# Performance work log

Measured on AMD Instinct MI355X. Metric: run time of the kernel, lower is better.

## Reference

```python
import jax, jax.numpy as jnp
import numpy as np

B, L, D_IN, D_EDGE, H, D = 2, 384, 256, 128, 8, 32
SCALE = D ** (-0.5)


def setup_inputs() -> dict:
    key = jax.random.key(0)
    ks = jax.random.split(key, 12)
    hd = H * D
    s_in = D_IN ** -0.5
    s_e = D_EDGE ** -0.5
    return {
        "node_feat": jax.random.normal(ks[0], (B, L, D_IN), jnp.float32),
        "edge_feat": jax.random.normal(ks[1], (B, L, L, D_EDGE), jnp.float32),
        "edge_mask": (jax.random.uniform(ks[2], (B, L, L)) > 0.15).astype(jnp.float32),
        "Wq": jax.random.normal(ks[3], (D_IN, hd), jnp.float32) * s_in,
        "bq": jnp.zeros((hd,), jnp.float32),
        "Wk": jax.random.normal(ks[4], (D_IN, hd), jnp.float32) * s_in,
        "bk": jnp.zeros((hd,), jnp.float32),
        "Wv": jax.random.normal(ks[5], (D_IN, hd), jnp.float32) * s_in,
        "bv": jnp.zeros((hd,), jnp.float32),
        "We": jax.random.normal(ks[6], (D_EDGE, hd), jnp.float32) * s_e,
        "Wu": jax.random.normal(ks[7], (D_IN, hd), jnp.float32) * s_in,
        "bu": jnp.zeros((hd,), jnp.float32),
    }


def _split_heads(t):
    # (b, l, h*d) -> (b, h, l, d)
    b, l, _ = t.shape
    return t.reshape(b, l, H, D).transpose(0, 2, 1, 3)


def reference(node_feat, edge_feat, edge_mask, Wq, bq, Wk, bk, Wv, bv, We, Wu, bu):
    q = _split_heads(node_feat @ Wq + bq)
    k = _split_heads(node_feat @ Wk + bk)
    v = _split_heads(node_feat @ Wv + bv)
    # edge embedding: (b, i, j, h*d) -> (b, h, i, j, d)
    b, l = edge_feat.shape[0], edge_feat.shape[1]
    e = (edge_feat @ We).reshape(b, l, l, H, D).transpose(0, 3, 1, 2, 4)
    logit = jnp.einsum('bhid,bhjd->bhij', q, k)
    logit = logit + jnp.einsum('bhid,bhijd->bhij', q, e)
    att = logit * SCALE
    att = att + ((1.0 - edge_mask) * -1e9)[:, None, :, :]
    att = jax.nn.softmax(att, axis=-1)  # dropout is identity in eval / p=0
    updated = jnp.einsum('bhij,bhjd->bhid', att, v)
    updated = updated + jnp.einsum('bhij,bhijd->bhid', att, e)
    updated = updated.transpose(0, 2, 1, 3).reshape(b, l, H * D)
    return (node_feat @ Wu + bu) + updated
```

## Files before the change

kernel.cpp:

```cpp
#include <hip/hip_runtime.h>
#include <cstdint>

#define NB 2
#define LL 384
#define DIN 256
#define DE 128
#define NH 8
#define DH 32
#define HD 256
#define SCALE 0.17677669529663687f

typedef __attribute__((ext_vector_type(8))) short bf16x8;
typedef __attribute__((ext_vector_type(4))) float f32x4;

static __device__ __forceinline__ unsigned short f2bf(float f) {
    uint32_t u = __builtin_bit_cast(uint32_t, f);
    u += 0x7FFF + ((u >> 16) & 1);
    return (unsigned short)(u >> 16);
}
static __device__ __forceinline__ float bf2f(unsigned short u) {
    return __builtin_bit_cast(float, (uint32_t)u << 16);
}
static __device__ __forceinline__ float getf4(const float4& v, int k) {
    return k == 0 ? v.x : k == 1 ? v.y : k == 2 ? v.z : v.w;
}
static __device__ __forceinline__ bf16x8 pack8(const float4& a, const float4& b) {
    bf16x8 p;
    p[0]=(short)f2bf(a.x); p[1]=(short)f2bf(a.y); p[2]=(short)f2bf(a.z); p[3]=(short)f2bf(a.w);
    p[4]=(short)f2bf(b.x); p[5]=(short)f2bf(b.y); p[6]=(short)f2bf(b.z); p[7]=(short)f2bf(b.w);
    return p;
}

__global__ __launch_bounds__(128) void prep_we(const float* __restrict__ We,
                                               unsigned short* __restrict__ WeT) {
    const int n = blockIdx.x;
    const int k = threadIdx.x;
    WeT[n * DE + k] = f2bf(We[(size_t)k * HD + n]);
}

__global__ __launch_bounds__(256) void proj_kernel(
    const float* __restrict__ node,
    const float* __restrict__ Wq, const float* __restrict__ bq,
    const float* __restrict__ Wk, const float* __restrict__ bk,
    const float* __restrict__ Wv, const float* __restrict__ bv,
    const float* __restrict__ Wu, const float* __restrict__ bu,
    unsigned short* __restrict__ qb16, unsigned short* __restrict__ kb16,
    float* __restrict__ vb, float* __restrict__ ub)
{
    __shared__ __align__(16) float rows[4][DIN];
    const int t  = threadIdx.x;
    const int r0 = blockIdx.x * 4;

    #pragma unroll
    for (int r = 0; r < 4; ++r)
        rows[r][t] = node[(size_t)(r0 + r) * DIN + t];
    __syncthreads();

    float aq[4], ak[4], av[4], au[4];
    {
        const float vq = bq[t], vk = bk[t], vv = bv[t], vu = bu[t];
        #pragma unroll
        for (int r = 0; r < 4; ++r) { aq[r] = vq; ak[r] = vk; av[r] = vv; au[r] = vu; }
    }

    for (int f4 = 0; f4 < DIN / 4; ++f4) {
        float4 xv[4];
        #pragma unroll
        for (int r = 0; r < 4; ++r)
            xv[r] = *(const float4*)&rows[r][f4 * 4];
        #pragma unroll
        for (int k = 0; k < 4; ++k) {
            const int f = f4 * 4 + k;
            const float wq = Wq[(size_t)f * HD + t];
            const float wk = Wk[(size_t)f * HD + t];
            const float wv = Wv[(size_t)f * HD + t];
            const float wu = Wu[(size_t)f * HD + t];
            #pragma unroll
            for (int r = 0; r < 4; ++r) {
                const float x = getf4(xv[r], k);
                aq[r] += x * wq; ak[r] += x * wk; av[r] += x * wv; au[r] += x * wu;
            }
        }
    }

    #pragma unroll
    for (int r = 0; r < 4; ++r) {
        const size_t o = (size_t)(r0 + r) * HD + t;
        qb16[o] = f2bf(aq[r]); kb16[o] = f2bf(ak[r]);
        vb[o] = av[r]; ub[o] = au[r];
    }
}

__global__ __launch_bounds__(256) void vt_kernel(const float* __restrict__ vb,
                                                 unsigned short* __restrict__ vT) {
    __shared__ float tile[64][65];
    int blk = blockIdx.x;
    const int b  = blk / 24; blk %= 24;
    const int jt = blk / 4;
    const int ct = blk % 4;
    const int j0 = jt * 64, c0 = ct * 64;
    const int t  = threadIdx.x;
    const int c  = t & 63, j4 = t >> 6;
    #pragma unroll
    for (int rr = 0; rr < 16; ++rr) {
        const int j = j4 + 4 * rr;
        tile[j][c] = vb[(size_t)(b * LL + j0 + j) * HD + c0 + c];
    }
    __syncthreads();
    const int jj = t & 63, c4 = t >> 6;
    #pragma unroll
    for (int rr = 0; rr < 16; ++rr) {
        const int cc = c4 + 4 * rr;
        vT[(size_t)(b * HD + c0 + cc) * LL + j0 + jj] = f2bf(tile[jj][cc]);
    }
}

__global__ __launch_bounds__(256) void qk_kernel(
    const unsigned short* __restrict__ qb16, const unsigned short* __restrict__ kb16,
    const float* __restrict__ mask, float* __restrict__ logit_pre)
{
    int idx = blockIdx.x;
    const int jt = idx % 6; idx /= 6;
    const int it = idx % 6; idx /= 6;
    const int h  = idx % NH;
    const int b  = idx / NH;
    const int t    = threadIdx.x;
    const int lane = t & 63;
    const int w    = t >> 6;
    const int lid  = lane & 15;
    const int g    = lane >> 4;
    const int i0 = it * 64 + w * 16;
    const int j0 = jt * 64;

    const bf16x8 afr = *(const bf16x8*)&qb16[(size_t)(b * LL + i0 + lid) * HD + h * DH + g * 8];
    f32x4 acc[4];
    #pragma unroll
    for (int jj = 0; jj < 4; ++jj) {
        const bf16x8 bfrg = *(const bf16x8*)&kb16[(size_t)(b * LL + j0 + jj * 16 + lid) * HD + h * DH + g * 8];
        acc[jj] = __builtin_amdgcn_mfma_f32_16x16x32_bf16(afr, bfrg, (f32x4){0.f,0.f,0.f,0.f}, 0, 0, 0);
    }
    #pragma unroll
    for (int jj = 0; jj < 4; ++jj) {
        #pragma unroll
        for (int r = 0; r < 4; ++r) {
            const int i = i0 + 4 * g + r;
            const int j = j0 + jj * 16 + lid;
            const float lg = SCALE * acc[jj][r]
                           + (1.0f - mask[(size_t)(b * LL + i) * LL + j]) * -1e9f;
            logit_pre[((size_t)(b * NH + h) * LL + i) * LL + j] = lg;
        }
    }
}

__global__ __launch_bounds__(256) void qwe_kernel(
    const unsigned short* __restrict__ qb16, const unsigned short* __restrict__ WeT,
    unsigned short* __restrict__ qWe)
{
    const int bi = blockIdx.x;
    const int t  = threadIdx.x;
    const int h  = t >> 5;
    const int c0 = (t & 31) * 4;

    float qv[32];
    const unsigned short* qp = &qb16[(size_t)bi * HD + h * DH];
    #pragma unroll
    for (int d = 0; d < 32; ++d) qv[d] = bf2f(qp[d]);

    float acc0 = 0.f, acc1 = 0.f, acc2 = 0.f, acc3 = 0.f;
    #pragma unroll
    for (int d = 0; d < 32; ++d) {
        const ushort4 wt = *(const ushort4*)&WeT[(size_t)(h * DH + d) * DE + c0];
        acc0 += qv[d] * bf2f(wt.x); acc1 += qv[d] * bf2f(wt.y);
        acc2 += qv[d] * bf2f(wt.z); acc3 += qv[d] * bf2f(wt.w);
    }
    unsigned short* o = &qWe[(size_t)bi * (NH * DE) + h * DE + c0];
    o[0] = f2bf(SCALE * acc0); o[1] = f2bf(SCALE * acc1);
    o[2] = f2bf(SCALE * acc2); o[3] = f2bf(SCALE * acc3);
}

__global__ __launch_bounds__(256) void elog_kernel(
    const float* __restrict__ edge,
    const unsigned short* __restrict__ qWe,
    float* __restrict__ lpre)
{
    int idx = blockIdx.x;
    const int jt = idx % 3; idx /= 3;
    const int bi = idx;
    const int b = bi / LL, ii = bi % LL;
    const int t = threadIdx.x, lane = t & 63, w = t >> 6;
    const int lid = lane & 15, g = lane >> 4;
    const int hq = lid & 7;
    const int j0 = jt * 128 + w * 32;

    bf16x8 bfr[4];
    const unsigned short* qwp = &qWe[(size_t)bi * (NH * DE) + hq * DE];
    #pragma unroll
    for (int kt = 0; kt < 4; ++kt)
        bfr[kt] = *(const bf16x8*)&qwp[kt * 32 + g * 8];

    f32x4 acc[2];
    #pragma unroll
    for (int mt = 0; mt < 2; ++mt) {
        acc[mt] = (f32x4){0.f, 0.f, 0.f, 0.f};
        const float* ef = edge + ((size_t)bi * LL + j0 + mt * 16 + lid) * DE;
        #pragma unroll
        for (int kt = 0; kt < 4; ++kt) {
            const float4 x0 = *(const float4*)&ef[kt * 32 + g * 8];
            const float4 x1 = *(const float4*)&ef[kt * 32 + g * 8 + 4];
            acc[mt] = __builtin_amdgcn_mfma_f32_16x16x32_bf16(pack8(x0, x1), bfr[kt], acc[mt], 0, 0, 0);
        }
    }

    if (lid < 8) {
        float* lrow = lpre + ((size_t)(b * NH + hq) * LL + ii) * LL;
        #pragma unroll
        for (int mt = 0; mt < 2; ++mt) {
            float4* p4 = (float4*)&lrow[j0 + mt * 16 + 4 * g];
            float4 x = *p4;
            x.x += acc[mt][0]; x.y += acc[mt][1];
            x.z += acc[mt][2]; x.w += acc[mt][3];
            *p4 = x;
        }
    }
}

__global__ __launch_bounds__(256) void smax_kernel(
    const float* __restrict__ lpre, unsigned short* __restrict__ attb)
{
    const int t = threadIdx.x, lane = t & 63, w = t >> 6;
    const int row = blockIdx.x * 4 + w;
    const float* lr = lpre + (size_t)row * LL;

    float2 x[3];
    #pragma unroll
    for (int k = 0; k < 3; ++k)
        x[k] = *(const float2*)&lr[2 * lane + 128 * k];

    float m = fmaxf(x[0].x, x[0].y);
    m = fmaxf(m, fmaxf(x[1].x, x[1].y));
    m = fmaxf(m, fmaxf(x[2].x, x[2].y));
    #pragma unroll
    for (int off = 1; off < 64; off <<= 1) m = fmaxf(m, __shfl_xor(m, off));

    float p[6], s = 0.f;
    #pragma unroll
    for (int k = 0; k < 3; ++k) {
        p[2 * k]     = __expf(x[k].x - m);
        p[2 * k + 1] = __expf(x[k].y - m);
        s += p[2 * k] + p[2 * k + 1];
    }
    #pragma unroll
    for (int off = 1; off < 64; off <<= 1) s += __shfl_xor(s, off);
    const float inv = 1.0f / s;

    unsigned int* ao = (unsigned int*)attb + (size_t)row * (LL / 2);
    #pragma unroll
    for (int k = 0; k < 3; ++k) {
        const unsigned int pk = ((unsigned int)f2bf(p[2 * k + 1] * inv) << 16)
                              |  (unsigned int)f2bf(p[2 * k] * inv);
        ao[lane + 64 * k] = pk;
    }
}

__global__ __launch_bounds__(512, 4) void pvs_kernel(
    const float* __restrict__ edge,
    const unsigned short* __restrict__ attb,
    const unsigned short* __restrict__ vT,
    float* __restrict__ aEp,
    float* __restrict__ avp)
{
    int idx = blockIdx.x;
    const int jt = idx % 3; idx /= 3;
    const int bi = idx;
    const int b = bi / LL, ii = bi % LL;
    const int t = threadIdx.x, lane = t & 63, w = t >> 6;
    const int lid = lane & 15, g = lane >> 4;
    const int h = lid & 7;
    const int j0 = jt * 128;

    bf16x8 pA[4];
    const unsigned short* ab = attb + ((size_t)(b * NH + h) * LL + ii) * LL + j0;
    #pragma unroll
    for (int kt = 0; kt < 4; ++kt)
        pA[kt] = *(const bf16x8*)&ab[kt * 32 + g * 8];

    const float* Eb = edge + ((size_t)bi * LL + j0) * DE + w * 16 + lid;
    f32x4 accE = (f32x4){0.f, 0.f, 0.f, 0.f};
    #pragma unroll
    for (int kt = 0; kt < 4; ++kt) {
        bf16x8 be;
        #pragma unroll
        for (int u = 0; u < 8; ++u)
            be[u] = (short)f2bf(Eb[(size_t)(kt * 32 + g * 8 + u) * DE]);
        accE = __builtin_amdgcn_mfma_f32_16x16x32_bf16(pA[kt], be, accE, 0, 0, 0);
    }

    f32x4 accV[2];
    accV[0] = (f32x4){0.f, 0.f, 0.f, 0.f};
    accV[1] = (f32x4){0.f, 0.f, 0.f, 0.f};
    #pragma unroll
    for (int kt = 0; kt < 4; ++kt) {
        #pragma unroll
        for (int mt = 0; mt < 2; ++mt) {
            const bf16x8 vv = *(const bf16x8*)&vT[(size_t)(b * HD + w * DH + mt * 16 + lid) * LL + j0 + kt * 32 + g * 8];
            accV[mt] = __builtin_amdgcn_mfma_f32_16x16x32_bf16(pA[kt], vv, accV[mt], 0, 0, 0);
        }
    }

    float* aep = aEp + (size_t)(bi * 3 + jt) * (NH * DE);
    if (g < 2) {
        #pragma unroll
        for (int r = 0; r < 4; ++r)
            aep[(4 * g + r) * DE + w * 16 + lid] = accE[r];
    }
    float* avo = avp + (size_t)(bi * 3 + jt) * HD;
    #pragma unroll
    for (int mt = 0; mt < 2; ++mt)
        #pragma unroll
        for (int r = 0; r < 4; ++r)
            if (4 * g + r == w)
                avo[w * DH + mt * 16 + lid] = accV[mt][r];
}

__global__ __launch_bounds__(256) void finale_kernel(
    const float* __restrict__ aEp, const float* __restrict__ avp,
    const float* __restrict__ We,
    const float* __restrict__ ub,
    float* __restrict__ out)
{
    __shared__ float aEs[NH * DE];
    const int bi = blockIdx.x, t = threadIdx.x;

    #pragma unroll
    for (int q = 0; q < 4; ++q) {
        const int x = t + 256 * q;
        aEs[x] = aEp[(size_t)(bi * 3 + 0) * (NH * DE) + x]
               + aEp[(size_t)(bi * 3 + 1) * (NH * DE) + x]
               + aEp[(size_t)(bi * 3 + 2) * (NH * DE) + x];
    }
    __syncthreads();

    const int hd = t, h = hd >> 5;
    float acc = ub[(size_t)bi * HD + hd]
              + avp[(size_t)(bi * 3 + 0) * HD + hd]
              + avp[(size_t)(bi * 3 + 1) * HD + hd]
              + avp[(size_t)(bi * 3 + 2) * HD + hd];

    const float* sa = &aEs[h * DE];
    float a0 = 0.f, a1 = 0.f, a2 = 0.f, a3 = 0.f;
    #pragma unroll
    for (int c = 0; c < DE; c += 4) {
        a0 += sa[c]     * We[(size_t)(c)     * HD + hd];
        a1 += sa[c + 1] * We[(size_t)(c + 1) * HD + hd];
        a2 += sa[c + 2] * We[(size_t)(c + 2) * HD + hd];
        a3 += sa[c + 3] * We[(size_t)(c + 3) * HD + hd];
    }
    out[(size_t)bi * HD + hd] = acc + ((a0 + a1) + (a2 + a3));
}

extern "C" void kernel_launch(void* const* d_in, const int* in_sizes, int n_in,
                              void* d_out, int out_size, void* d_ws, size_t ws_size,
                              hipStream_t stream) {
    const float* node = (const float*)d_in[0];
    const float* edge = (const float*)d_in[1];
    const float* mask = (const float*)d_in[2];
    const float* Wq   = (const float*)d_in[3];
    const float* bq   = (const float*)d_in[4];
    const float* Wk   = (const float*)d_in[5];
    const float* bk   = (const float*)d_in[6];
    const float* Wv   = (const float*)d_in[7];
    const float* bv   = (const float*)d_in[8];
    const float* We   = (const float*)d_in[9];
    const float* Wu   = (const float*)d_in[10];
    const float* bu   = (const float*)d_in[11];
    float* out = (float*)d_out;

    const size_t rowsz = (size_t)NB * LL * HD;
    const size_t lsz   = (size_t)NB * NH * LL * LL;
    float* ws   = (float*)d_ws;
    float* vb   = ws;
    float* ubuf = vb + rowsz;
    float* lpre = ubuf + rowsz;
    float* aEp  = lpre + lsz;
    float* avp  = aEp + (size_t)NB * LL * 3 * NH * DE;
    unsigned short* us   = (unsigned short*)(avp + (size_t)NB * LL * 3 * HD);
    unsigned short* WeT  = us;
    unsigned short* qb16 = WeT + (size_t)HD * DE;
    unsigned short* kb16 = qb16 + rowsz;
    unsigned short* vT   = kb16 + rowsz;
    unsigned short* qWeB = vT + rowsz;
    unsigned short* attb = qWeB + (size_t)NB * LL * NH * DE;

    hipLaunchKernelGGL(prep_we, dim3(HD), dim3(DE), 0, stream, We, WeT);
    hipLaunchKernelGGL(proj_kernel, dim3(NB * LL / 4), dim3(256), 0, stream,
                       node, Wq, bq, Wk, bk, Wv, bv, Wu, bu, qb16, kb16, vb, ubuf);
    hipLaunchKernelGGL(vt_kernel, dim3(NB * (LL / 64) * (HD / 64)), dim3(256), 0, stream,
                       vb, vT);
    hipLaunchKernelGGL(qk_kernel, dim3(NB * NH * (LL / 64) * (LL / 64)), dim3(256), 0, stream,
                       qb16, kb16, mask, lpre);
    hipLaunchKernelGGL(qwe_kernel, dim3(NB * LL), dim3(256), 0, stream,
                       qb16, WeT, qWeB);
    hipLaunchKernelGGL(elog_kernel, dim3(NB * LL * 3), dim3(256), 0, stream,
                       edge, qWeB, lpre);
    hipLaunchKernelGGL(smax_kernel, dim3(NB * NH * LL / 4), dim3(256), 0, stream,
                       lpre, attb);
    hipLaunchKernelGGL(pvs_kernel, dim3(NB * LL * 3), dim3(512), 0, stream,
                       edge, attb, vT, aEp, avp);
    hipLaunchKernelGGL(finale_kernel, dim3(NB * LL), dim3(256), 0, stream,
                       aEp, avp, We, ubuf, out);
}
```

Baseline: 121.9 us.

## Emit transposed bf16 edge copy in logit kernel; read it in PV kernel

The edge-logit kernel now converts each edge tile to bf16, transposes it through swizzled shared memory, and writes a j-contiguous bf16 copy to workspace. The PV kernel then reads this half-size, coalesced copy instead of re-reading fp32 edge features with strided scalar loads. The PV kernel also drops to 256 threads, with each wave computing more output tiles, and the qk logit load is hoisted before the MFMAs. This trades an extra 75 MB-class bf16 write plus 32 KB of shared memory per block for a cheaper second pass over the edge tensor.

```diff
diff --git a/kernel.cpp b/kernel.cpp
--- a/kernel.cpp
+++ b/kernel.cpp
@@ -178,48 +178,88 @@
     o[2] = f2bf(SCALE * acc2); o[3] = f2bf(SCALE * acc3);
 }
 
-__global__ __launch_bounds__(256) void elog_kernel(
+__global__ __launch_bounds__(256, 2) void elog2_kernel(
     const float* __restrict__ edge,
     const unsigned short* __restrict__ qWe,
-    float* __restrict__ lpre)
-{
-    int idx = blockIdx.x;
-    const int jt = idx % 3; idx /= 3;
-    const int bi = idx;
+    float* __restrict__ lpre,
+    unsigned short* __restrict__ ebfT)
+{
+    __shared__ __align__(16) unsigned short ET[DE * DE];
+
+    int blk = blockIdx.x;
+    const int jt = blk % 3; const int bi = blk / 3;
     const int b = bi / LL, ii = bi % LL;
     const int t = threadIdx.x, lane = t & 63, w = t >> 6;
     const int lid = lane & 15, g = lane >> 4;
-    const int hq = lid & 7;
+    const int h8 = lid & 7;
     const int j0 = jt * 128 + w * 32;
 
-    bf16x8 bfr[4];
-    const unsigned short* qwp = &qWe[(size_t)bi * (NH * DE) + hq * DE];
-    #pragma unroll
-    for (int kt = 0; kt < 4; ++kt)
-        bfr[kt] = *(const bf16x8*)&qwp[kt * 32 + g * 8];
+    float4 eL[2][4][2];
+    #pragma unroll
+    for (int mt = 0; mt < 2; ++mt) {
+        const float* ef = edge + ((size_t)bi * LL + j0 + mt * 16 + lid) * DE;
+        #pragma unroll
+        for (int kt = 0; kt < 4; ++kt) {
+            eL[mt][kt][0] = *(const float4*)&ef[kt * 32 + g * 8];
+            eL[mt][kt][1] = *(const float4*)&ef[kt * 32 + g * 8 + 4];
+        }
+    }
+    bf16x8 qfr[4];
+    {
+        const unsigned short* qwp = &qWe[(size_t)bi * (NH * DE) + h8 * DE];
+        #pragma unroll
+        for (int kt = 0; kt < 4; ++kt)
+            qfr[kt] = *(const bf16x8*)&qwp[kt * 32 + g * 8];
+    }
+    float* lrow = lpre + ((size_t)(b * NH + h8) * LL + ii) * LL;
+    float4 qk4[2];
+    #pragma unroll
+    for (int mt = 0; mt < 2; ++mt)
+        qk4[mt] = *(const float4*)&lrow[j0 + mt * 16 + 4 * g];
 
     f32x4 acc[2];
     #pragma unroll
     for (int mt = 0; mt < 2; ++mt) {
         acc[mt] = (f32x4){0.f, 0.f, 0.f, 0.f};
-        const float* ef = edge + ((size_t)bi * LL + j0 + mt * 16 + lid) * DE;
+        const int jl = w * 32 + mt * 16 + lid;
+        const int jhi = (jl >> 4) ;
         #pragma unroll
         for (int kt = 0; kt < 4; ++kt) {
-            const float4 x0 = *(const float4*)&ef[kt * 32 + g * 8];
-            const float4 x1 = *(const float4*)&ef[kt * 32 + g * 8 + 4];
-            acc[mt] = __builtin_amdgcn_mfma_f32_16x16x32_bf16(pack8(x0, x1), bfr[kt], acc[mt], 0, 0, 0);
+            const bf16x8 pk = pack8(eL[mt][kt][0], eL[mt][kt][1]);
+            #pragma unroll
+            for (int u = 0; u < 8; ++u) {
+                const int c = kt * 32 + g * 8 + u;
+                const int swz = (c ^ (c >> 3)) & 7;
+                ET[c * DE + ((jhi ^ swz) << 4) + (jl & 15)] = (unsigned short)pk[u];
+            }
+            acc[mt] = __builtin_amdgcn_mfma_f32_16x16x32_bf16(pk, qfr[kt], acc[mt], 0, 0, 0);
         }
     }
 
     if (lid < 8) {
-        float* lrow = lpre + ((size_t)(b * NH + hq) * LL + ii) * LL;
         #pragma unroll
         for (int mt = 0; mt < 2; ++mt) {
-            float4* p4 = (float4*)&lrow[j0 + mt * 16 + 4 * g];
-            float4 x = *p4;
+            float4 x = qk4[mt];
             x.x += acc[mt][0]; x.y += acc[mt][1];
             x.z += acc[mt][2]; x.w += acc[mt][3];
-            *p4 = x;
+            *(float4*)&lrow[j0 + mt * 16 + 4 * g] = x;
+        }
+    }
+
+    __syncthreads();
+
+    #pragma unroll
+    for (int s = 0; s < 2; ++s) {
+        const int c = w * 32 + s * 16 + lid;
+        const int swz = (c ^ (c >> 3)) & 7;
+        unsigned short* dst = &ebfT[((size_t)bi * DE + c) * LL + jt * 128];
+        const unsigned short* src = &ET[c * DE];
+        #pragma unroll
+        for (int it = 0; it < 4; ++it) {
+            const int p   = it * 4 + g;
+            const int j16 = p >> 1, hl = p & 1;
+            const bf16x8 v = *(const bf16x8*)&src[((j16 ^ swz) << 4) + hl * 8];
+            *(bf16x8*)&dst[j16 * 16 + hl * 8] = v;
         }
     }
 }
@@ -262,64 +302,82 @@
     }
 }
 
-__global__ __launch_bounds__(512, 4) void pvs_kernel(
-    const float* __restrict__ edge,
+__global__ __launch_bounds__(256, 2) void pv2_kernel(
+    const unsigned short* __restrict__ ebfT,
     const unsigned short* __restrict__ attb,
     const unsigned short* __restrict__ vT,
     float* __restrict__ aEp,
     float* __restrict__ avp)
 {
-    int idx = blockIdx.x;
-    const int jt = idx % 3; idx /= 3;
-    const int bi = idx;
+    int blk = blockIdx.x;
+    const int jt = blk % 3; const int bi = blk / 3;
     const int b = bi / LL, ii = bi % LL;
     const int t = threadIdx.x, lane = t & 63, w = t >> 6;
     const int lid = lane & 15, g = lane >> 4;
-    const int h = lid & 7;
+    const int h8 = lid & 7;
     const int j0 = jt * 128;
 
     bf16x8 pA[4];
-    const unsigned short* ab = attb + ((size_t)(b * NH + h) * LL + ii) * LL + j0;
-    #pragma unroll
-    for (int kt = 0; kt < 4; ++kt)
-        pA[kt] = *(const bf16x8*)&ab[kt * 32 + g * 8];
-
-    const float* Eb = edge + ((size_t)bi * LL + j0) * DE + w * 16 + lid;
-    f32x4 accE = (f32x4){0.f, 0.f, 0.f, 0.f};
-    #pragma unroll
-    for (int kt = 0; kt < 4; ++kt) {
-        bf16x8 be;
-        #pragma unroll
-        for (int u = 0; u < 8; ++u)
-            be[u] = (short)f2bf(Eb[(size_t)(kt * 32 + g * 8 + u) * DE]);
-        accE = __builtin_amdgcn_mfma_f32_16x16x32_bf16(pA[kt], be, accE, 0, 0, 0);
-    }
-
-    f32x4 accV[2];
-    accV[0] = (f32x4){0.f, 0.f, 0.f, 0.f};
-    accV[1] = (f32x4){0.f, 0.f, 0.f, 0.f};
-    #pragma unroll
-    for (int kt = 0; kt < 4; ++kt) {
-        #pragma unroll
-        for (int mt = 0; mt < 2; ++mt) {
-            const bf16x8 vv = *(const bf16x8*)&vT[(size_t)(b * HD + w * DH + mt * 16 + lid) * LL + j0 + kt * 32 + g * 8];
-            accV[mt] = __builtin_amdgcn_mfma_f32_16x16x32_bf16(pA[kt], vv, accV[mt], 0, 0, 0);
-        }
+    {
+        const unsigned short* ab = attb + ((size_t)(b * NH + h8) * LL + ii) * LL + j0;
+        #pragma unroll
+        for (int kt = 0; kt < 4; ++kt)
+            pA[kt] = *(const bf16x8*)&ab[kt * 32 + g * 8];
+    }
+
+    bf16x8 be[2][4];
+    #pragma unroll
+    for (int ct = 0; ct < 2; ++ct) {
+        const unsigned short* er = &ebfT[((size_t)bi * DE + 32 * w + ct * 16 + lid) * LL + j0];
+        #pragma unroll
+        for (int kt = 0; kt < 4; ++kt)
+            be[ct][kt] = *(const bf16x8*)&er[kt * 32 + g * 8];
+    }
+    bf16x8 vv[4][4];
+    #pragma unroll
+    for (int nt = 0; nt < 4; ++nt) {
+        const unsigned short* vr = &vT[((size_t)b * HD + 64 * w + nt * 16 + lid) * LL + j0];
+        #pragma unroll
+        for (int kt = 0; kt < 4; ++kt)
+            vv[nt][kt] = *(const bf16x8*)&vr[kt * 32 + g * 8];
+    }
+
+    f32x4 accE[2];
+    #pragma unroll
+    for (int ct = 0; ct < 2; ++ct) {
+        accE[ct] = (f32x4){0.f, 0.f, 0.f, 0.f};
+        #pragma unroll
+        for (int kt = 0; kt < 4; ++kt)
+            accE[ct] = __builtin_amdgcn_mfma_f32_16x16x32_bf16(pA[kt], be[ct][kt], accE[ct], 0, 0, 0);
+    }
+    f32x4 accV[4];
+    #pragma unroll
+    for (int nt = 0; nt < 4; ++nt) {
+        accV[nt] = (f32x4){0.f, 0.f, 0.f, 0.f};
+        #pragma unroll
+        for (int kt = 0; kt < 4; ++kt)
+            accV[nt] = __builtin_amdgcn_mfma_f32_16x16x32_bf16(pA[kt], vv[nt][kt], accV[nt], 0, 0, 0);
     }
 
     float* aep = aEp + (size_t)(bi * 3 + jt) * (NH * DE);
     if (g < 2) {
         #pragma unroll
-        for (int r = 0; r < 4; ++r)
-            aep[(4 * g + r) * DE + w * 16 + lid] = accE[r];
+        for (int ct = 0; ct < 2; ++ct)
+            #pragma unroll
+            for (int r = 0; r < 4; ++r)
+                aep[(4 * g + r) * DE + 32 * w + ct * 16 + lid] = accE[ct][r];
     }
     float* avo = avp + (size_t)(bi * 3 + jt) * HD;
     #pragma unroll
-    for (int mt = 0; mt < 2; ++mt)
-        #pragma unroll
-        for (int r = 0; r < 4; ++r)
-            if (4 * g + r == w)
-                avo[w * DH + mt * 16 + lid] = accV[mt][r];
+    for (int nt = 0; nt < 4; ++nt) {
+        const int h = 2 * w + (nt >> 1);
+        if (g == (h >> 2)) {
+            const int r = h & 3;
+            const float val = r == 0 ? accV[nt][0] : r == 1 ? accV[nt][1]
+                            : r == 2 ? accV[nt][2] : accV[nt][3];
+            avo[64 * w + nt * 16 + lid] = val;
+        }
+    }
 }
 
 __global__ __launch_bounds__(256) void finale_kernel(
@@ -390,6 +448,7 @@
     unsigned short* vT   = kb16 + rowsz;
     unsigned short* qWeB = vT + rowsz;
     unsigned short* attb = qWeB + (size_t)NB * LL * NH * DE;
+    unsigned short* ebfT = attb + lsz;
 
     hipLaunchKernelGGL(prep_we, dim3(HD), dim3(DE), 0, stream, We, WeT);
     hipLaunchKernelGGL(proj_kernel, dim3(NB * LL / 4), dim3(256), 0, stream,
@@ -400,12 +459,12 @@
                        qb16, kb16, mask, lpre);
     hipLaunchKernelGGL(qwe_kernel, dim3(NB * LL), dim3(256), 0, stream,
                        qb16, WeT, qWeB);
-    hipLaunchKernelGGL(elog_kernel, dim3(NB * LL * 3), dim3(256), 0, stream,
-                       edge, qWeB, lpre);
+    hipLaunchKernelGGL(elog2_kernel, dim3(NB * LL * 3), dim3(256), 0, stream,
+                       edge, qWeB, lpre, ebfT);
     hipLaunchKernelGGL(smax_kernel, dim3(NB * NH * LL / 4), dim3(256), 0, stream,
                        lpre, attb);
-    hipLaunchKernelGGL(pvs_kernel, dim3(NB * LL * 3), dim3(512), 0, stream,
-                       edge, attb, vT, aEp, avp);
+    hipLaunchKernelGGL(pv2_kernel, dim3(NB * LL * 3), dim3(256), 0, stream,
+                       ebfT, attb, vT, aEp, avp);
     hipLaunchKernelGGL(finale_kernel, dim3(NB * LL), dim3(256), 0, stream,
                        aEp, avp, We, ubuf, out);
 }
```

New measurement: 139.4 us. 1.14x slower.

## Split pvs into fp32 edge-attention and MFMA att·V kernels, drop partial sums

Applied to the files above, without the earlier changes.

Replaces the combined pvs kernel, which split j into three tiles and wrote partial results, with two kernels that each handle a full row. aek_kernel does att·E in fp32 with coalesced float2 edge loads and attention staged in LDS. avk_kernel does att·V with MFMA over all 384 j. Softmax now also writes an fp32 attention copy. elog loads edge and logits up front to hide latency. The aim is coalesced strided edge reads, no bf16 conversion of E, and a simpler finale, at the cost of extra attention traffic and a second full pass over the edge tensor.

```diff
diff --git a/kernel.cpp b/kernel.cpp
--- a/kernel.cpp
+++ b/kernel.cpp
@@ -178,7 +178,7 @@
     o[2] = f2bf(SCALE * acc2); o[3] = f2bf(SCALE * acc3);
 }
 
-__global__ __launch_bounds__(256) void elog_kernel(
+__global__ __launch_bounds__(256, 2) void elog_kernel(
     const float* __restrict__ edge,
     const unsigned short* __restrict__ qWe,
     float* __restrict__ lpre)
@@ -192,40 +192,55 @@
     const int hq = lid & 7;
     const int j0 = jt * 128 + w * 32;
 
-    bf16x8 bfr[4];
-    const unsigned short* qwp = &qWe[(size_t)bi * (NH * DE) + hq * DE];
-    #pragma unroll
-    for (int kt = 0; kt < 4; ++kt)
-        bfr[kt] = *(const bf16x8*)&qwp[kt * 32 + g * 8];
+    float4 eL[2][4][2];
+    #pragma unroll
+    for (int mt = 0; mt < 2; ++mt) {
+        const float* ef = edge + ((size_t)bi * LL + j0 + mt * 16 + lid) * DE;
+        #pragma unroll
+        for (int kt = 0; kt < 4; ++kt) {
+            eL[mt][kt][0] = *(const float4*)&ef[kt * 32 + g * 8];
+            eL[mt][kt][1] = *(const float4*)&ef[kt * 32 + g * 8 + 4];
+        }
+    }
+    float* lrow = lpre + ((size_t)(b * NH + hq) * LL + ii) * LL;
+    float4 qk4[2];
+    #pragma unroll
+    for (int mt = 0; mt < 2; ++mt)
+        qk4[mt] = *(const float4*)&lrow[j0 + mt * 16 + 4 * g];
+
+    bf16x8 qfr[4];
+    {
+        const unsigned short* qwp = &qWe[(size_t)bi * (NH * DE) + hq * DE];
+        #pragma unroll
+        for (int kt = 0; kt < 4; ++kt)
+            qfr[kt] = *(const bf16x8*)&qwp[kt * 32 + g * 8];
+    }
 
     f32x4 acc[2];
     #pragma unroll
     for (int mt = 0; mt < 2; ++mt) {
         acc[mt] = (f32x4){0.f, 0.f, 0.f, 0.f};
-        const float* ef = edge + ((size_t)bi * LL + j0 + mt * 16 + lid) * DE;
         #pragma unroll
         for (int kt = 0; kt < 4; ++kt) {
-            const float4 x0 = *(const float4*)&ef[kt * 32 + g * 8];
-            const float4 x1 = *(const float4*)&ef[kt * 32 + g * 8 + 4];
-            acc[mt] = __builtin_amdgcn_mfma_f32_16x16x32_bf16(pack8(x0, x1), bfr[kt], acc[mt], 0, 0, 0);
+            const bf16x8 pk = pack8(eL[mt][kt][0], eL[mt][kt][1]);
+            acc[mt] = __builtin_amdgcn_mfma_f32_16x16x32_bf16(pk, qfr[kt], acc[mt], 0, 0, 0);
         }
     }
 
     if (lid < 8) {
-        float* lrow = lpre + ((size_t)(b * NH + hq) * LL + ii) * LL;
         #pragma unroll
         for (int mt = 0; mt < 2; ++mt) {
-            float4* p4 = (float4*)&lrow[j0 + mt * 16 + 4 * g];
-            float4 x = *p4;
+            float4 x = qk4[mt];
             x.x += acc[mt][0]; x.y += acc[mt][1];
             x.z += acc[mt][2]; x.w += acc[mt][3];
-            *p4 = x;
+            *(float4*)&lrow[j0 + mt * 16 + 4 * g] = x;
         }
     }
 }
 
 __global__ __launch_bounds__(256) void smax_kernel(
-    const float* __restrict__ lpre, unsigned short* __restrict__ attb)
+    const float* __restrict__ lpre,
+    unsigned short* __restrict__ attb, float* __restrict__ attf)
 {
     const int t = threadIdx.x, lane = t & 63, w = t >> 6;
     const int row = blockIdx.x * 4 + w;
@@ -254,76 +269,90 @@
     const float inv = 1.0f / s;
 
     unsigned int* ao = (unsigned int*)attb + (size_t)row * (LL / 2);
+    float* af = attf + (size_t)row * LL;
     #pragma unroll
     for (int k = 0; k < 3; ++k) {
-        const unsigned int pk = ((unsigned int)f2bf(p[2 * k + 1] * inv) << 16)
-                              |  (unsigned int)f2bf(p[2 * k] * inv);
+        const float p0 = p[2 * k] * inv, p1 = p[2 * k + 1] * inv;
+        const unsigned int pk = ((unsigned int)f2bf(p1) << 16) | (unsigned int)f2bf(p0);
         ao[lane + 64 * k] = pk;
-    }
-}
-
-__global__ __launch_bounds__(512, 4) void pvs_kernel(
+        *(float2*)&af[2 * lane + 128 * k] = (float2){p0, p1};
+    }
+}
+
+__global__ __launch_bounds__(512, 2) void aek_kernel(
     const float* __restrict__ edge,
+    const float* __restrict__ attf,
+    float* __restrict__ aEq)
+{
+    __shared__ float ps[NH][LL];
+    const int bi = blockIdx.x, b = bi / LL, ii = bi % LL;
+    const int t = threadIdx.x, lane = t & 63, w = t >> 6;
+
+    {
+        const float* ar = attf + ((size_t)(b * NH + w) * LL + ii) * LL;
+        #pragma unroll
+        for (int k = 0; k < 3; ++k)
+            *(float2*)&ps[w][2 * lane + 128 * k] = *(const float2*)&ar[2 * lane + 128 * k];
+    }
+    __syncthreads();
+
+    const float* eb = edge + (size_t)bi * LL * DE + 2 * lane;
+    float2 acc = {0.f, 0.f};
+    #pragma unroll 2
+    for (int j = 0; j < LL; j += 4) {
+        const float4 pv = *(const float4*)&ps[w][j];
+        const float2 e0 = *(const float2*)&eb[(size_t)(j + 0) * DE];
+        const float2 e1 = *(const float2*)&eb[(size_t)(j + 1) * DE];
+        const float2 e2 = *(const float2*)&eb[(size_t)(j + 2) * DE];
+        const float2 e3 = *(const float2*)&eb[(size_t)(j + 3) * DE];
+        acc.x += pv.x * e0.x; acc.y += pv.x * e0.y;
+        acc.x += pv.y * e1.x; acc.y += pv.y * e1.y;
+        acc.x += pv.z * e2.x; acc.y += pv.z * e2.y;
+        acc.x += pv.w * e3.x; acc.y += pv.w * e3.y;
+    }
+    *(float2*)&aEq[(size_t)bi * (NH * DE) + w * DE + 2 * lane] = acc;
+}
+
+__global__ __launch_bounds__(256, 2) void avk_kernel(
     const unsigned short* __restrict__ attb,
     const unsigned short* __restrict__ vT,
-    float* __restrict__ aEp,
-    float* __restrict__ avp)
-{
-    int idx = blockIdx.x;
-    const int jt = idx % 3; idx /= 3;
-    const int bi = idx;
-    const int b = bi / LL, ii = bi % LL;
+    float* __restrict__ avq)
+{
+    const int bi = blockIdx.x, b = bi / LL, ii = bi % LL;
     const int t = threadIdx.x, lane = t & 63, w = t >> 6;
     const int lid = lane & 15, g = lane >> 4;
-    const int h = lid & 7;
-    const int j0 = jt * 128;
-
-    bf16x8 pA[4];
-    const unsigned short* ab = attb + ((size_t)(b * NH + h) * LL + ii) * LL + j0;
-    #pragma unroll
-    for (int kt = 0; kt < 4; ++kt)
-        pA[kt] = *(const bf16x8*)&ab[kt * 32 + g * 8];
-
-    const float* Eb = edge + ((size_t)bi * LL + j0) * DE + w * 16 + lid;
-    f32x4 accE = (f32x4){0.f, 0.f, 0.f, 0.f};
-    #pragma unroll
-    for (int kt = 0; kt < 4; ++kt) {
-        bf16x8 be;
-        #pragma unroll
-        for (int u = 0; u < 8; ++u)
-            be[u] = (short)f2bf(Eb[(size_t)(kt * 32 + g * 8 + u) * DE]);
-        accE = __builtin_amdgcn_mfma_f32_16x16x32_bf16(pA[kt], be, accE, 0, 0, 0);
-    }
-
-    f32x4 accV[2];
-    accV[0] = (f32x4){0.f, 0.f, 0.f, 0.f};
-    accV[1] = (f32x4){0.f, 0.f, 0.f, 0.f};
-    #pragma unroll
-    for (int kt = 0; kt < 4; ++kt) {
-        #pragma unroll
-        for (int mt = 0; mt < 2; ++mt) {
-            const bf16x8 vv = *(const bf16x8*)&vT[(size_t)(b * HD + w * DH + mt * 16 + lid) * LL + j0 + kt * 32 + g * 8];
-            accV[mt] = __builtin_amdgcn_mfma_f32_16x16x32_bf16(pA[kt], vv, accV[mt], 0, 0, 0);
-        }
-    }
-
-    float* aep = aEp + (size_t)(bi * 3 + jt) * (NH * DE);
-    if (g < 2) {
-        #pragma unroll
-        for (int r = 0; r < 4; ++r)
-            aep[(4 * g + r) * DE + w * 16 + lid] = accE[r];
-    }
-    float* avo = avp + (size_t)(bi * 3 + jt) * HD;
-    #pragma unroll
-    for (int mt = 0; mt < 2; ++mt)
-        #pragma unroll
-        for (int r = 0; r < 4; ++r)
-            if (4 * g + r == w)
-                avo[w * DH + mt * 16 + lid] = accV[mt][r];
+    const int h8 = lid & 7;
+
+    bf16x8 pA[12];
+    {
+        const unsigned short* ab = attb + ((size_t)(b * NH + h8) * LL + ii) * LL;
+        #pragma unroll
+        for (int kt = 0; kt < 12; ++kt)
+            pA[kt] = *(const bf16x8*)&ab[kt * 32 + g * 8];
+    }
+
+    const unsigned short* vTb = vT + (size_t)b * HD * LL;
+    #pragma unroll
+    for (int nt = 0; nt < 4; ++nt) {
+        const int hd = 64 * w + nt * 16 + lid;
+        const unsigned short* vr = &vTb[(size_t)hd * LL];
+        f32x4 acc = (f32x4){0.f, 0.f, 0.f, 0.f};
+        #pragma unroll
+        for (int kt = 0; kt < 12; ++kt) {
+            const bf16x8 vv = *(const bf16x8*)&vr[kt * 32 + g * 8];
+            acc = __builtin_amdgcn_mfma_f32_16x16x32_bf16(pA[kt], vv, acc, 0, 0, 0);
+        }
+        const int h = 2 * w + (nt >> 1);
+        if (g == (h >> 2)) {
+            const int r = h & 3;
+            const float val = r == 0 ? acc[0] : r == 1 ? acc[1] : r == 2 ? acc[2] : acc[3];
+            avq[(size_t)bi * HD + hd] = val;
+        }
+    }
 }
 
 __global__ __launch_bounds__(256) void finale_kernel(
-    const float* __restrict__ aEp, const float* __restrict__ avp,
+    const float* __restrict__ aEq, const float* __restrict__ avq,
     const float* __restrict__ We,
     const float* __restrict__ ub,
     float* __restrict__ out)
@@ -332,19 +361,12 @@
     const int bi = blockIdx.x, t = threadIdx.x;
 
     #pragma unroll
-    for (int q = 0; q < 4; ++q) {
-        const int x = t + 256 * q;
-        aEs[x] = aEp[(size_t)(bi * 3 + 0) * (NH * DE) + x]
-               + aEp[(size_t)(bi * 3 + 1) * (NH * DE) + x]
-               + aEp[(size_t)(bi * 3 + 2) * (NH * DE) + x];
-    }
+    for (int q = 0; q < 4; ++q)
+        aEs[t + 256 * q] = aEq[(size_t)bi * (NH * DE) + t + 256 * q];
     __syncthreads();
 
     const int hd = t, h = hd >> 5;
-    float acc = ub[(size_t)bi * HD + hd]
-              + avp[(size_t)(bi * 3 + 0) * HD + hd]
-              + avp[(size_t)(bi * 3 + 1) * HD + hd]
-              + avp[(size_t)(bi * 3 + 2) * HD + hd];
+    float acc = ub[(size_t)bi * HD + hd] + avq[(size_t)bi * HD + hd];
 
     const float* sa = &aEs[h * DE];
     float a0 = 0.f, a1 = 0.f, a2 = 0.f, a3 = 0.f;
@@ -381,9 +403,10 @@
     float* vb   = ws;
     float* ubuf = vb + rowsz;
     float* lpre = ubuf + rowsz;
-    float* aEp  = lpre + lsz;
-    float* avp  = aEp + (size_t)NB * LL * 3 * NH * DE;
-    unsigned short* us   = (unsigned short*)(avp + (size_t)NB * LL * 3 * HD);
+    float* attf = lpre + lsz;
+    float* aEq  = attf + lsz;
+    float* avq  = aEq + (size_t)NB * LL * NH * DE;
+    unsigned short* us   = (unsigned short*)(avq + rowsz);
     unsigned short* WeT  = us;
     unsigned short* qb16 = WeT + (size_t)HD * DE;
     unsigned short* kb16 = qb16 + rowsz;
@@ -403,9 +426,11 @@
     hipLaunchKernelGGL(elog_kernel, dim3(NB * LL * 3), dim3(256), 0, stream,
                        edge, qWeB, lpre);
     hipLaunchKernelGGL(smax_kernel, dim3(NB * NH * LL / 4), dim3(256), 0, stream,
-                       lpre, attb);
-    hipLaunchKernelGGL(pvs_kernel, dim3(NB * LL * 3), dim3(512), 0, stream,
-                       edge, attb, vT, aEp, avp);
+                       lpre, attb, attf);
+    hipLaunchKernelGGL(aek_kernel, dim3(NB * LL), dim3(512), 0, stream,
+                       edge, attf, aEq);
+    hipLaunchKernelGGL(avk_kernel, dim3(NB * LL), dim3(256), 0, stream,
+                       attb, vT, avq);
     hipLaunchKernelGGL(finale_kernel, dim3(NB * LL), dim3(256), 0, stream,
-                       aEp, avp, We, ubuf, out);
-}
+                       aEq, avq, We, ubuf, out);
+}
```

After: 179.0 us. 1.47x slower.
